# Performance work log

Hardware: AMD Instinct MI355X
Metric: run time of the kernel (lower is better)

The kernel has to match this reference:

```python
import jax, jax.numpy as jnp
import numpy as np

EMB_DIM = 128
DEC_DIM = 128
NEG_INF = -1e10


def setup_inputs() -> dict:
    key = jax.random.key(0)
    k1, k2, k3, k4, k5, k6 = jax.random.split(key, 6)
    B, S = 64, 4096
    hidden = jax.random.normal(k1, (B, DEC_DIM), dtype=jnp.float32)
    seq_embs = jax.random.normal(k2, (S, B, EMB_DIM), dtype=jnp.float32)
    mask = jax.random.randint(k3, (B, S), 0, 2, dtype=jnp.int32)
    # nn.Linear(emb_dim + dec_dim, dec_dim): weight [dec_dim, emb_dim+dec_dim]
    fan_in = EMB_DIM + DEC_DIM
    bound = 1.0 / np.sqrt(fan_in)
    W_attn = jax.random.uniform(k4, (DEC_DIM, fan_in), minval=-bound, maxval=bound, dtype=jnp.float32)
    b_attn = jax.random.uniform(k5, (DEC_DIM,), minval=-bound, maxval=bound, dtype=jnp.float32)
    # nn.Linear(dec_dim, 1, bias=False): weight [1, dec_dim]
    bound_v = 1.0 / np.sqrt(DEC_DIM)
    v_w = jax.random.uniform(k6, (1, DEC_DIM), minval=-bound_v, maxval=bound_v, dtype=jnp.float32)
    return {"hidden": hidden, "seq_embs": seq_embs, "mask": mask,
            "W_attn": W_attn, "b_attn": b_attn, "v_w": v_w}


def reference(hidden, seq_embs, mask, W_attn, b_attn, v_w):
    # hidden: [B, Dd]; seq_embs: [S, B, De]; mask: [B, S]
    # Concat order in torch is (hidden, seq_embs) -> split W accordingly.
    Wh = W_attn[:, :DEC_DIM]   # [Dd, Dd] applied to hidden
    We = W_attn[:, DEC_DIM:]   # [Dd, De] applied to seq_embs
    embs = jnp.transpose(seq_embs, (1, 0, 2))            # [B, S, De]
    # energy = tanh(Linear(cat(hidden, embs))) without materializing concat
    h_proj = hidden @ Wh.T + b_attn                       # [B, Dd]
    e_proj = jnp.einsum('bse,de->bsd', embs, We)          # [B, S, Dd]
    energy = jnp.tanh(h_proj[:, None, :] + e_proj)        # [B, S, Dd]
    attention = jnp.einsum('bsd,d->bs', energy, v_w[0])   # [B, S]
    attention = jnp.where(mask == 0, NEG_INF, attention)
    return jax.nn.softmax(attention, axis=1)
```

## Files before the change

### kernel.cpp

```cpp
#include <hip/hip_runtime.h>
#include <hip/hip_bf16.h>

#define BB 64
#define SS 4096
#define EE 128
#define DD 128
#define FAN 256
#define TILES 4
#define ROWS (TILES * 64)
#define NEG_INF_F (-1e10f)

typedef __bf16 bf16x8 __attribute__((ext_vector_type(8)));
typedef unsigned short u16x8 __attribute__((ext_vector_type(8)));
typedef float f32x4 __attribute__((ext_vector_type(4)));

__device__ inline bf16x8 ld_frag_lds(const unsigned char* p) {
    union { u16x8 u; bf16x8 b; } c;
    c.u = *(const u16x8*)p;
    return c.b;
}

__device__ inline uint2 f4_to_bf4(float4 f) {
    union { __hip_bfloat162 b; unsigned u; } lo, hi;
    lo.b = __float22bfloat162_rn(make_float2(f.x, f.y));
    hi.b = __float22bfloat162_rn(make_float2(f.z, f.w));
    return make_uint2(lo.u, hi.u);
}

__device__ inline float tanh_fast(float x) {
    float ax = fabsf(x);
    float e = __expf(-2.0f * ax);
    float t = (1.0f - e) * __builtin_amdgcn_rcpf(1.0f + e);
    return x < 0.0f ? -t : t;
}

__global__ __launch_bounds__(256) void prep_kernel(
        const float* __restrict__ hidden, const float* __restrict__ W_attn,
        const float* __restrict__ b_attn, const float* __restrict__ v_w,
        float* __restrict__ hproj, unsigned char* __restrict__ Wb,
        float* __restrict__ v_out) {
    const int b = blockIdx.x;
    const int t = threadIdx.x;
    if (t < 128) {
        float acc = b_attn[t];
        const float4* hrow = (const float4*)(hidden + b * DD);
        const float4* wrow = (const float4*)(W_attn + t * FAN);
        #pragma unroll
        for (int e = 0; e < 32; e++) {
            float4 h = hrow[e], w = wrow[e];
            acc += h.x * w.x + h.y * w.y + h.z * w.z + h.w * w.w;
        }
        hproj[b * DD + t] = acc;
        if (b == 0) v_out[t] = v_w[t];
    } else {
        int tt = t - 128;
        int d  = 2 * b + (tt >> 6);
        int e0 = (tt & 63) * 2;
        float2 src = *(const float2*)(W_attn + d * FAN + DD + e0);
        union { __hip_bfloat162 bb; unsigned u; } c;
        c.bb = __float22bfloat162_rn(src);
        unsigned off = (unsigned)(d * 256)
                     + (((unsigned)(e0 * 2)) ^ (((unsigned)d & 7u) << 4));
        *(unsigned*)(Wb + off) = c.u;
    }
}

__global__ __launch_bounds__(256, 4) void logits_kernel(
        const float* __restrict__ seq_embs, const int* __restrict__ mask,
        const float* __restrict__ hproj, const unsigned char* __restrict__ Wb,
        const float* __restrict__ v, float* __restrict__ out,
        float* __restrict__ psums) {
    __shared__ __attribute__((aligned(1024))) unsigned char Ws[DD * EE * 2];

    const int b    = blockIdx.y;
    const int g    = blockIdx.x;
    const int tid  = threadIdx.x;
    const int wave = tid >> 6;
    const int lane = tid & 63;
    const int m    = lane & 15;
    const int quad = lane >> 4;
    const int arow = wave * 16 + m;

    #pragma unroll
    for (int j = 0; j < 8; j++) {
        const int c = wave * 8 + j;
        __builtin_amdgcn_global_load_lds(
            (const __attribute__((address_space(1))) unsigned int*)(Wb + c * 1024 + lane * 16),
            (__attribute__((address_space(3))) unsigned int*)(Ws + c * 1024),
            16, 0, 0);
    }

    const int* __restrict__ mask_g = mask + (size_t)b * SS + g * ROWS;
    const float* __restrict__ xbase = seq_embs
        + (size_t)(g * ROWS + arow) * (BB * EE)
        + (size_t)b * EE + quad * 8;

    int am[2];
    int4 mq[2];
    bf16x8 af[2][4];
    {
        am[0] = mask_g[arow];
        mq[0] = *(const int4*)(mask_g + wave * 16 + quad * 4);
        const float* xrow = xbase;
        #pragma unroll
        for (int kk = 0; kk < 4; kk++) {
            union { uint4 q; bf16x8 bf; } c;
            c.q = make_uint4(0u, 0u, 0u, 0u);
            if (am[0] != 0) {
                float4 f0 = *(const float4*)(xrow + kk * 32);
                float4 f1 = *(const float4*)(xrow + kk * 32 + 4);
                uint2 a = f4_to_bf4(f0), bq = f4_to_bf4(f1);
                c.q = make_uint4(a.x, a.y, bq.x, bq.y);
            }
            af[0][kk] = c.bf;
        }
    }

    float hp_r[8], v_r[8];
    #pragma unroll
    for (int t = 0; t < 8; t++) {
        hp_r[t] = hproj[b * DD + t * 16 + m];
        v_r[t]  = v[t * 16 + m];
    }

    __syncthreads();

    const unsigned sw = ((unsigned)(m & 7)) << 4;
    float blocksum = 0.0f;

    #pragma unroll
    for (int tile = 0; tile < TILES; tile++) {
        const int cur = tile & 1;
        if (tile + 1 < TILES) {
            const int nxt = cur ^ 1;
            am[nxt] = mask_g[(tile + 1) * 64 + arow];
            mq[nxt] = *(const int4*)(mask_g + (tile + 1) * 64 + wave * 16 + quad * 4);
            const float* xrow = xbase + (size_t)((tile + 1) * 64) * (BB * EE);
            #pragma unroll
            for (int kk = 0; kk < 4; kk++) {
                union { uint4 q; bf16x8 bf; } c;
                c.q = make_uint4(0u, 0u, 0u, 0u);
                if (am[nxt] != 0) {
                    float4 f0 = *(const float4*)(xrow + kk * 32);
                    float4 f1 = *(const float4*)(xrow + kk * 32 + 4);
                    uint2 a = f4_to_bf4(f0), bq = f4_to_bf4(f1);
                    c.q = make_uint4(a.x, a.y, bq.x, bq.y);
                }
                af[nxt][kk] = c.bf;
            }
        }

        f32x4 acc[8];
        #pragma unroll
        for (int t = 0; t < 8; t++) acc[t] = (f32x4){0.f, 0.f, 0.f, 0.f};
        #pragma unroll
        for (int kk = 0; kk < 4; kk++) {
            const unsigned cb = ((unsigned)(kk * 64 + quad * 16)) ^ sw;
            #pragma unroll
            for (int t = 0; t < 8; t++) {
                bf16x8 bf = ld_frag_lds(Ws + (unsigned)((t * 16 + m) * 256) + cb);
                acc[t] = __builtin_amdgcn_mfma_f32_16x16x32_bf16(af[cur][kk], bf, acc[t], 0, 0, 0);
            }
        }

        const int mqa[4] = {mq[cur].x, mq[cur].y, mq[cur].z, mq[cur].w};
        float red[4];
        #pragma unroll
        for (int r = 0; r < 4; r++) {
            float red_r = 0.0f;
            if (mqa[r] != 0) {
                float part = 0.f;
                #pragma unroll
                for (int t = 0; t < 8; t++)
                    part += v_r[t] * tanh_fast(hp_r[t] + acc[t][r]);
                part += __shfl_xor(part, 1);
                part += __shfl_xor(part, 2);
                part += __shfl_xor(part, 4);
                part += __shfl_xor(part, 8);
                red_r = __expf(part);
            }
            red[r] = red_r;
            blocksum += red_r;
        }
        if (m == 0) {
            *(float4*)&out[(size_t)b * SS + g * ROWS + tile * 64
                           + wave * 16 + quad * 4] =
                make_float4(red[0], red[1], red[2], red[3]);
        }
    }

    blocksum += __shfl_xor(blocksum, 16);
    blocksum += __shfl_xor(blocksum, 32);
    if (lane == 0) psums[(b * 16 + g) * 4 + wave] = blocksum;
}

__global__ __launch_bounds__(256) void norm_kernel(
        float* __restrict__ out, const float* __restrict__ psums) {
    const int b = blockIdx.y;
    const int tid = threadIdx.x;
    const int lane = tid & 63;
    float p = psums[b * 64 + lane];
    #pragma unroll
    for (int off = 32; off >= 1; off >>= 1)
        p += __shfl_xor(p, off);
    const float inv = 1.0f / p;
    const int i = (blockIdx.x * 256 + tid) * 4;
    float4 v = *(float4*)&out[(size_t)b * SS + i];
    v.x *= inv; v.y *= inv; v.z *= inv; v.w *= inv;
    *(float4*)&out[(size_t)b * SS + i] = v;
}

extern "C" void kernel_launch(void* const* d_in, const int* in_sizes, int n_in,
                              void* d_out, int out_size, void* d_ws, size_t ws_size,
                              hipStream_t stream) {
    const float* hidden   = (const float*)d_in[0];
    const float* seq_embs = (const float*)d_in[1];
    const int*   mask     = (const int*)d_in[2];
    const float* W_attn   = (const float*)d_in[3];
    const float* b_attn   = (const float*)d_in[4];
    const float* v_w      = (const float*)d_in[5];
    float* out = (float*)d_out;

    float*         hproj = (float*)d_ws;
    unsigned char* Wb    = (unsigned char*)d_ws + 32768;
    float*         vv    = (float*)((char*)d_ws + 65536);
    float*         psums = (float*)((char*)d_ws + 66048);

    prep_kernel<<<64, 256, 0, stream>>>(hidden, W_attn, b_attn, v_w, hproj, Wb, vv);
    dim3 grid(SS / ROWS, BB);
    logits_kernel<<<grid, 256, 0, stream>>>(seq_embs, mask, hproj, Wb, vv, out, psums);
    dim3 ngrid(SS / (256 * 4), BB);
    norm_kernel<<<ngrid, 256, 0, stream>>>(out, psums);
}
```

Baseline: 211.4 us.

## Keep bf16 weight fragments in registers instead of LDS, double rows per block

Each wave now loads its MFMA B-operand fragments for the whole 128x128 bf16 weight matrix straight from global memory into 128 VGPRs. These fragments are reused across all tiles, which removes the LDS staging, the XOR swizzle, the block barrier and the per-tile LDS reads. The weight layout is now plain row-major. Each block now covers 8 tiles of 64 rows, so the grid halves and the partial-sum count per batch drops to 32, which the normalisation kernel follows. The cost is much higher register pressure (launch bounds lowered to 2 blocks per SIMD-unit target), fewer resident waves to hide seq_embs load latency, and duplicated weight reads from L2 by every wave.

```diff
diff --git a/kernel.cpp b/kernel.cpp
--- a/kernel.cpp
+++ b/kernel.cpp
@@ -6,15 +6,14 @@
 #define EE 128
 #define DD 128
 #define FAN 256
-#define TILES 4
+#define TILES 8
 #define ROWS (TILES * 64)
-#define NEG_INF_F (-1e10f)
 
 typedef __bf16 bf16x8 __attribute__((ext_vector_type(8)));
 typedef unsigned short u16x8 __attribute__((ext_vector_type(8)));
 typedef float f32x4 __attribute__((ext_vector_type(4)));
 
-__device__ inline bf16x8 ld_frag_lds(const unsigned char* p) {
+__device__ inline bf16x8 ld_frag(const unsigned short* p) {
     union { u16x8 u; bf16x8 b; } c;
     c.u = *(const u16x8*)p;
     return c.b;
@@ -37,7 +36,7 @@
 __global__ __launch_bounds__(256) void prep_kernel(
         const float* __restrict__ hidden, const float* __restrict__ W_attn,
         const float* __restrict__ b_attn, const float* __restrict__ v_w,
-        float* __restrict__ hproj, unsigned char* __restrict__ Wb,
+        float* __restrict__ hproj, unsigned short* __restrict__ Wb,
         float* __restrict__ v_out) {
     const int b = blockIdx.x;
     const int t = threadIdx.x;
@@ -59,19 +58,15 @@
         float2 src = *(const float2*)(W_attn + d * FAN + DD + e0);
         union { __hip_bfloat162 bb; unsigned u; } c;
         c.bb = __float22bfloat162_rn(src);
-        unsigned off = (unsigned)(d * 256)
-                     + (((unsigned)(e0 * 2)) ^ (((unsigned)d & 7u) << 4));
-        *(unsigned*)(Wb + off) = c.u;
-    }
-}
-
-__global__ __launch_bounds__(256, 4) void logits_kernel(
+        *(unsigned*)&Wb[d * EE + e0] = c.u;
+    }
+}
+
+__global__ __launch_bounds__(256, 2) void logits_kernel(
         const float* __restrict__ seq_embs, const int* __restrict__ mask,
-        const float* __restrict__ hproj, const unsigned char* __restrict__ Wb,
+        const float* __restrict__ hproj, const unsigned short* __restrict__ Wb,
         const float* __restrict__ v, float* __restrict__ out,
         float* __restrict__ psums) {
-    __shared__ __attribute__((aligned(1024))) unsigned char Ws[DD * EE * 2];
-
     const int b    = blockIdx.y;
     const int g    = blockIdx.x;
     const int tid  = threadIdx.x;
@@ -81,14 +76,12 @@
     const int quad = lane >> 4;
     const int arow = wave * 16 + m;
 
-    #pragma unroll
-    for (int j = 0; j < 8; j++) {
-        const int c = wave * 8 + j;
-        __builtin_amdgcn_global_load_lds(
-            (const __attribute__((address_space(1))) unsigned int*)(Wb + c * 1024 + lane * 16),
-            (__attribute__((address_space(3))) unsigned int*)(Ws + c * 1024),
-            16, 0, 0);
-    }
+    bf16x8 bw[4][8];
+    #pragma unroll
+    for (int kk = 0; kk < 4; kk++)
+        #pragma unroll
+        for (int t = 0; t < 8; t++)
+            bw[kk][t] = ld_frag(Wb + (t * 16 + m) * EE + kk * 32 + quad * 8);
 
     const int* __restrict__ mask_g = mask + (size_t)b * SS + g * ROWS;
     const float* __restrict__ xbase = seq_embs
@@ -123,9 +116,6 @@
         v_r[t]  = v[t * 16 + m];
     }
 
-    __syncthreads();
-
-    const unsigned sw = ((unsigned)(m & 7)) << 4;
     float blocksum = 0.0f;
 
     #pragma unroll
@@ -155,12 +145,9 @@
         for (int t = 0; t < 8; t++) acc[t] = (f32x4){0.f, 0.f, 0.f, 0.f};
         #pragma unroll
         for (int kk = 0; kk < 4; kk++) {
-            const unsigned cb = ((unsigned)(kk * 64 + quad * 16)) ^ sw;
             #pragma unroll
-            for (int t = 0; t < 8; t++) {
-                bf16x8 bf = ld_frag_lds(Ws + (unsigned)((t * 16 + m) * 256) + cb);
-                acc[t] = __builtin_amdgcn_mfma_f32_16x16x32_bf16(af[cur][kk], bf, acc[t], 0, 0, 0);
-            }
+            for (int t = 0; t < 8; t++)
+                acc[t] = __builtin_amdgcn_mfma_f32_16x16x32_bf16(af[cur][kk], bw[kk][t], acc[t], 0, 0, 0);
         }
 
         const int mqa[4] = {mq[cur].x, mq[cur].y, mq[cur].z, mq[cur].w};
@@ -191,17 +178,16 @@
 
     blocksum += __shfl_xor(blocksum, 16);
     blocksum += __shfl_xor(blocksum, 32);
-    if (lane == 0) psums[(b * 16 + g) * 4 + wave] = blocksum;
+    if (lane == 0) psums[(b * 8 + g) * 4 + wave] = blocksum;
 }
 
 __global__ __launch_bounds__(256) void norm_kernel(
         float* __restrict__ out, const float* __restrict__ psums) {
     const int b = blockIdx.y;
     const int tid = threadIdx.x;
-    const int lane = tid & 63;
-    float p = psums[b * 64 + lane];
-    #pragma unroll
-    for (int off = 32; off >= 1; off >>= 1)
+    float p = psums[b * 32 + (tid & 31)];
+    #pragma unroll
+    for (int off = 16; off >= 1; off >>= 1)
         p += __shfl_xor(p, off);
     const float inv = 1.0f / p;
     const int i = (blockIdx.x * 256 + tid) * 4;
@@ -221,10 +207,10 @@
     const float* v_w      = (const float*)d_in[5];
     float* out = (float*)d_out;
 
-    float*         hproj = (float*)d_ws;
-    unsigned char* Wb    = (unsigned char*)d_ws + 32768;
-    float*         vv    = (float*)((char*)d_ws + 65536);
-    float*         psums = (float*)((char*)d_ws + 66048);
+    float*          hproj = (float*)d_ws;
+    unsigned short* Wb    = (unsigned short*)((char*)d_ws + 32768);
+    float*          vv    = (float*)((char*)d_ws + 65536);
+    float*          psums = (float*)((char*)d_ws + 66048);
 
     prep_kernel<<<64, 256, 0, stream>>>(hidden, W_attn, b_attn, v_w, hproj, Wb, vv);
     dim3 grid(SS / ROWS, BB);
```

Result: slower. 227.0 us (+7.4%).
